# Performance work log

Hardware: AMD Instinct MI355X
Metric: run time of the kernel (lower is better)

The kernel has to match this reference:

```python
import jax, jax.numpy as jnp
import numpy as np
from jax import lax

B, CIN, H, W = 64, 3, 224, 224
FEAT = 64          # conv output channels after pooling
OUT = 1024         # output_dim


def _conv2d(x, w, b, stride):
    # x: NCHW, w: OIHW, padding=1, stride=stride
    y = lax.conv_general_dilated(
        x, w, window_strides=(stride, stride), padding=((1, 1), (1, 1)),
        dimension_numbers=("NCHW", "OIHW", "NCHW"))
    return y + b[None, :, None, None]


def setup_inputs() -> dict:
    key = jax.random.key(0)
    ks = jax.random.split(key, 12)
    s = 0.05
    return {
        "x": jax.random.normal(ks[0], (B, CIN, H, W), dtype=jnp.float32),
        "w1": jax.random.normal(ks[1], (32, CIN, 3, 3), dtype=jnp.float32) * s,
        "b1": jax.random.normal(ks[2], (32,), dtype=jnp.float32) * s,
        "w2": jax.random.normal(ks[3], (64, 32, 3, 3), dtype=jnp.float32) * s,
        "b2": jax.random.normal(ks[4], (64,), dtype=jnp.float32) * s,
        "wm": jax.random.normal(ks[5], (OUT, FEAT), dtype=jnp.float32) * s,
        "bm": jax.random.normal(ks[6], (OUT,), dtype=jnp.float32) * s,
        "wc": jax.random.normal(ks[7], (OUT, FEAT * FEAT), dtype=jnp.float32) * s,
        "bc": jax.random.normal(ks[8], (OUT,), dtype=jnp.float32) * s,
        "w3": jax.random.normal(ks[9], (OUT, FEAT ** 3), dtype=jnp.float32) * s,
        "b3": jax.random.normal(ks[10], (OUT,), dtype=jnp.float32) * s,
    }


def reference(x, w1, b1, w2, b2, wm, bm, wc, bc, w3, b3):
    # conv trunk: conv3x3 s2 -> relu -> conv3x3 s2 -> relu -> global avg pool
    h = jax.nn.relu(_conv2d(x, w1, b1, 2))
    h = jax.nn.relu(_conv2d(h, w2, b2, 2))
    feat = jnp.mean(h, axis=(2, 3))                    # (B, 64)

    mean_feat = feat @ wm.T + bm                       # (B, OUT)

    fc = feat - jnp.mean(feat, axis=1, keepdims=True)  # centered (B, 64)

    # 2nd-order: outer product flattened -> linear
    cov = (fc[:, :, None] * fc[:, None, :]).reshape(B, FEAT * FEAT)
    cov_feat = cov @ wc.T + bc

    # 3rd-order: rank-1 third-order outer product flattened -> linear
    outer3 = (fc[:, :, None, None] * fc[:, None, :, None] * fc[:, None, None, :])
    third_feat = outer3.reshape(B, FEAT ** 3) @ w3.T + b3

    return mean_feat + cov_feat + third_feat
```

## Files before the change

### kernel.cpp

```cpp
#include <hip/hip_runtime.h>
#include <hip/hip_bf16.h>

#define BB   64
#define CIN  3
#define HH   224
#define WW   224
#define C1   32
#define H1   112
#define W1   112
#define C2   64
#define H2   56
#define W2   56
#define FEATN 64
#define OUTN 1024
#define K3TOT (FEATN*FEATN*FEATN)

typedef __bf16 bf16x8 __attribute__((ext_vector_type(8)));
typedef float  f32x4  __attribute__((ext_vector_type(4)));
typedef unsigned int u32;

__device__ __forceinline__ void gload_lds16(const void* g, void* l) {
  __builtin_amdgcn_global_load_lds((const __attribute__((address_space(1))) u32*)g,
                                   (__attribute__((address_space(3))) u32*)l, 16, 0, 0);
}
__device__ __forceinline__ void gload_lds16_nt(const void* g, void* l) {
  __builtin_amdgcn_global_load_lds((const __attribute__((address_space(1))) u32*)g,
                                   (__attribute__((address_space(3))) u32*)l, 16, 0, 2);
}

__global__ __launch_bounds__(256) void prep_kernel(__bf16* __restrict__ h1T,
        const float* __restrict__ w2, __bf16* __restrict__ wf) {
    int gid = blockIdx.x * 256 + threadIdx.x;
    if (gid < 64 * 452) {
      int b = gid / 452, s = gid - b * 452;
      int row, col;
      if      (s < 114) { row = 0;        col = s; }
      else if (s < 228) { row = 113;      col = s - 114; }
      else if (s < 340) { row = s - 227;  col = 0; }
      else              { row = s - 339;  col = 113; }
      __bf16* p = h1T + (((size_t)b * 114 + row) * 114 + col) * 32;
      bf16x8 z = {};
      #pragma unroll
      for (int k = 0; k < 4; ++k) *(bf16x8*)(p + k * 8) = z;
    } else if (gid < 64 * 452 + 18432) {
      int t = gid - 64 * 452;
      int e    = t & 7;
      int lane = (t >> 3) & 63;
      int q    = (t >> 9) % 9;
      int j    = t / 4608;
      int oc = j * 16 + (lane & 15);
      int c  = (lane >> 4) * 8 + e;
      wf[t] = (__bf16)w2[(oc * C1 + c) * 9 + q];
    }
}

__global__ __launch_bounds__(256) void conv1_kernel(const float* __restrict__ x,
        const float* __restrict__ w1, const float* __restrict__ b1,
        __bf16* __restrict__ h1T) {
    int pos = blockIdx.x * 256 + threadIdx.x;
    int b   = pos / (H1 * 56);
    int rem = pos - b * (H1 * 56);
    int oy  = rem / 56;
    int g   = rem - oy * 56;
    int iy0 = oy * 2 - 1;

    float win[CIN][3][5];
    #pragma unroll
    for (int c = 0; c < CIN; ++c)
      #pragma unroll
      for (int dy = 0; dy < 3; ++dy) {
        int iy = iy0 + dy;
        bool rv = (iy >= 0) & (iy < HH);
        const float* row = x + ((size_t)(b * CIN + c) * HH + (rv ? iy : 0)) * WW;
        float lf = (rv && g > 0) ? row[4 * g - 1] : 0.f;
        float4 f4 = rv ? *(const float4*)(row + 4 * g) : (float4){0.f, 0.f, 0.f, 0.f};
        win[c][dy][0] = lf;
        win[c][dy][1] = f4.x; win[c][dy][2] = f4.y;
        win[c][dy][3] = f4.z; win[c][dy][4] = f4.w;
      }

    float acc[2][C1];
    #pragma unroll
    for (int u = 0; u < 2; ++u)
      #pragma unroll
      for (int oc = 0; oc < C1; ++oc) acc[u][oc] = b1[oc];

    #pragma unroll
    for (int c = 0; c < CIN; ++c)
      #pragma unroll
      for (int dy = 0; dy < 3; ++dy)
        #pragma unroll
        for (int dx = 0; dx < 3; ++dx) {
          float w0 = win[c][dy][dx];
          float w1v = win[c][dy][dx + 2];
          const float* wq = w1 + c * 9 + dy * 3 + dx;
          #pragma unroll
          for (int oc = 0; oc < C1; ++oc) {
            float wv = wq[oc * 27];
            acc[0][oc] = fmaf(wv, w0, acc[0][oc]);
            acc[1][oc] = fmaf(wv, w1v, acc[1][oc]);
          }
        }

    __bf16* dst = h1T + (((size_t)b * 114 + oy + 1) * 114 + (2 * g) + 1) * 32;
    #pragma unroll
    for (int u = 0; u < 2; ++u) {
      bf16x8 outv[4];
      #pragma unroll
      for (int k = 0; k < 32; ++k)
        outv[k >> 3][k & 7] = (__bf16)fmaxf(acc[u][k], 0.f);
      #pragma unroll
      for (int k = 0; k < 4; ++k) *(bf16x8*)(dst + u * 32 + k * 8) = outv[k];
    }
}

__global__ __launch_bounds__(256) void conv2_kernel(const __bf16* __restrict__ h1T,
        const __bf16* __restrict__ wf, const float* __restrict__ b2,
        float* __restrict__ featp) {
    __shared__ __align__(16) char tile[2304 * 16];
    __shared__ float pool_red[4][64];
    int t = threadIdx.x;
    int bid = blockIdx.x;
    int b  = bid / 28;
    int yt = bid - b * 28;
    int y0 = yt * 2;
    int w = t >> 6, lane = t & 63, l15 = lane & 15, l4 = lane >> 4;

    const char* src_base = (const char*)(h1T + ((size_t)b * 114 + 2 * y0) * 114 * 32);
    #pragma unroll
    for (int i = 0; i < 9; ++i) {
      int g = (w * 9 + i) * 64 + lane;
      int site = g >> 2; site = site < 569 ? site : 569;
      int qp = g & 3;
      int r5 = site / 114;
      int col = site - r5 * 114;
      int ql = (qp - col) & 3;
      gload_lds16(src_base + (size_t)site * 64 + ql * 16, tile + (size_t)g * 16);
    }
    __syncthreads();

    int sbase[2], urot[2];
    #pragma unroll
    for (int p = 0; p < 2; ++p) {
      int mt = 2 * w + p;
      int yl = mt >> 2;
      int xl = ((mt & 3) << 4) + l15;
      int xe = xl < 55 ? xl : 55;
      sbase[p] = ((yl * 2) * 114 + 2 * xe) * 64;
      urot[p]  = (l4 + 2 * xe) & 3;
    }

    f32x4 acc[2][4];
    #pragma unroll
    for (int p = 0; p < 2; ++p)
      #pragma unroll
      for (int j = 0; j < 4; ++j) acc[p][j] = (f32x4){0.f, 0.f, 0.f, 0.f};

    #pragma unroll
    for (int q = 0; q < 9; ++q) {
      int dy = q / 3, dx = q % 3;
      bf16x8 bw[4];
      #pragma unroll
      for (int j = 0; j < 4; ++j)
        bw[j] = *(const bf16x8*)(wf + ((j * 9 + q) * 64 + lane) * 8);
      bf16x8 af[2];
      #pragma unroll
      for (int p = 0; p < 2; ++p) {
        int addr = sbase[p] + (dy * 114 + dx) * 64 + (((urot[p] + dx) & 3) << 4);
        af[p] = *(const bf16x8*)(tile + addr);
      }
      #pragma unroll
      for (int p = 0; p < 2; ++p)
        #pragma unroll
        for (int j = 0; j < 4; ++j)
          acc[p][j] = __builtin_amdgcn_mfma_f32_16x16x32_bf16(af[p], bw[j], acc[p][j], 0, 0, 0);
    }

    float bias[4];
    #pragma unroll
    for (int j = 0; j < 4; ++j) bias[j] = b2[j * 16 + l15];
    float ps[4] = {0.f, 0.f, 0.f, 0.f};
    #pragma unroll
    for (int p = 0; p < 2; ++p) {
      int mt = 2 * w + p;
      bool valid = ((mt & 3) != 3) || (l4 < 2);
      #pragma unroll
      for (int j = 0; j < 4; ++j) {
        float sj = 0.f;
        #pragma unroll
        for (int r = 0; r < 4; ++r)
          sj += fmaxf(acc[p][j][r] + bias[j], 0.f);
        ps[j] += valid ? sj : 0.f;
      }
    }
    #pragma unroll
    for (int j = 0; j < 4; ++j) {
      ps[j] += __shfl_xor(ps[j], 16);
      ps[j] += __shfl_xor(ps[j], 32);
    }
    if (l4 == 0) {
      #pragma unroll
      for (int j = 0; j < 4; ++j) pool_red[w][j * 16 + l15] = ps[j];
    }
    __syncthreads();
    if (t < 64) {
      float s = pool_red[0][t] + pool_red[1][t] + pool_red[2][t] + pool_red[3][t];
      featp[((size_t)yt * 64 + b) * 64 + t] = s;
    }
}

__global__ __launch_bounds__(64) void center2_kernel(const float* __restrict__ featp,
        float* __restrict__ featN, float* __restrict__ fc) {
    int b = blockIdx.x;
    int c = threadIdx.x;
    float s = 0.f;
    #pragma unroll 7
    for (int yt = 0; yt < 28; ++yt)
      s += featp[((size_t)yt * 64 + b) * 64 + c];
    s *= (1.f / (H2 * W2));
    float tot = s;
    #pragma unroll
    for (int off = 32; off; off >>= 1) tot += __shfl_xor(tot, off);
    featN[b * 64 + c] = s;
    fc[b * 64 + c]    = s - tot * (1.f / 64.f);
}

#define T3_NCH 128

struct T3S {
    float stage[2][2][16][64];
    float fcT[64][66];
    float wred[2][64];
};

__global__ __launch_bounds__(128) void third_kernel(const float* __restrict__ fc,
        const float* __restrict__ w3, float* __restrict__ thrd) {
    __shared__ __align__(16) T3S sh;
    int t = threadIdx.x;
    int w = t >> 6, lane = t & 63, l15 = lane & 15, l4 = lane >> 4;
    int o = blockIdx.x;
    int swz = (l15 & 7) << 4;

    for (int idx = t; idx < 4096; idx += 128)
      sh.fcT[idx & 63][idx >> 6] = fc[idx];

    const char* seg = (const char*)w3 + ((size_t)o << 20) + (size_t)w * 524288;

    #pragma unroll
    for (int ii = 0; ii < 4; ++ii) {
      int row = ii * 4 + (lane >> 4);
      int lo  = (lane & 15) * 16;
      gload_lds16_nt(seg + row * 256 + (lo ^ ((row & 7) << 4)),
                     (char*)&sh.stage[w][0][0][0] + ii * 1024);
    }

    bf16x8 bfrag[2][4];
    #pragma unroll
    for (int ks = 0; ks < 2; ++ks)
      #pragma unroll
      for (int nt = 0; nt < 4; ++nt) {
        const float* p = fc + (nt * 16 + l15) * 64 + ks * 32 + l4 * 8;
        float4 v0 = *(const float4*)p;
        float4 v1 = *(const float4*)(p + 4);
        bfrag[ks][nt][0] = (__bf16)v0.x; bfrag[ks][nt][1] = (__bf16)v0.y;
        bfrag[ks][nt][2] = (__bf16)v0.z; bfrag[ks][nt][3] = (__bf16)v0.w;
        bfrag[ks][nt][4] = (__bf16)v1.x; bfrag[ks][nt][5] = (__bf16)v1.y;
        bfrag[ks][nt][6] = (__bf16)v1.z; bfrag[ks][nt][7] = (__bf16)v1.w;
      }

    __syncthreads();

    float oacc[4] = {0.f, 0.f, 0.f, 0.f};

    #pragma unroll 1
    for (int c = 0; c < T3_NCH; ++c) {
      if (c + 1 < T3_NCH) {
        const char* s2 = seg + (size_t)(c + 1) * 4096;
        char* db = (char*)&sh.stage[w][(c + 1) & 1][0][0];
        #pragma unroll
        for (int ii = 0; ii < 4; ++ii) {
          int row = ii * 4 + (lane >> 4);
          int lo  = (lane & 15) * 16;
          gload_lds16_nt(s2 + row * 256 + (lo ^ ((row & 7) << 4)), db + ii * 1024);
        }
        asm volatile("s_waitcnt vmcnt(4)" ::: "memory");
      } else {
        asm volatile("s_waitcnt vmcnt(0)" ::: "memory");
      }
      __builtin_amdgcn_sched_barrier(0);

      const char* cb = (const char*)&sh.stage[w][c & 1][0][0];
      f32x4 acc[4];
      #pragma unroll
      for (int nt = 0; nt < 4; ++nt) acc[nt] = (f32x4){0.f, 0.f, 0.f, 0.f};
      #pragma unroll
      for (int ks = 0; ks < 2; ++ks) {
        int off0 = l15 * 256 + ((ks * 128 + l4 * 32) ^ swz);
        float4 a0 = *(const float4*)(cb + off0);
        float4 a1 = *(const float4*)(cb + (off0 ^ 16));
        bf16x8 af;
        af[0] = (__bf16)a0.x; af[1] = (__bf16)a0.y;
        af[2] = (__bf16)a0.z; af[3] = (__bf16)a0.w;
        af[4] = (__bf16)a1.x; af[5] = (__bf16)a1.y;
        af[6] = (__bf16)a1.z; af[7] = (__bf16)a1.w;
        #pragma unroll
        for (int nt = 0; nt < 4; ++nt)
          acc[nt] = __builtin_amdgcn_mfma_f32_16x16x32_bf16(af, bfrag[ks][nt], acc[nt], 0, 0, 0);
      }
      int i = w * 32 + (c >> 2);
      #pragma unroll
      for (int nt = 0; nt < 4; ++nt) {
        int b = nt * 16 + l15;
        float s = 0.f;
        #pragma unroll
        for (int r = 0; r < 4; ++r) {
          int j = (c * 16 + l4 * 4 + r) & 63;
          s = fmaf(sh.fcT[j][b], acc[nt][r], s);
        }
        oacc[nt] = fmaf(sh.fcT[i][b], s, oacc[nt]);
      }
    }

    #pragma unroll
    for (int nt = 0; nt < 4; ++nt) {
      oacc[nt] += __shfl_xor(oacc[nt], 16);
      oacc[nt] += __shfl_xor(oacc[nt], 32);
    }
    if (l4 == 0) {
      #pragma unroll
      for (int nt = 0; nt < 4; ++nt) sh.wred[w][nt * 16 + l15] = oacc[nt];
    }
    __syncthreads();
    if (t < 64) thrd[o * 64 + t] = sh.wred[0][t] + sh.wred[1][t];
}

__global__ __launch_bounds__(256) void finale_kernel(const float* __restrict__ feat,
        const float* __restrict__ fc,
        const float* __restrict__ wm, const float* __restrict__ bm,
        const float* __restrict__ wc, const float* __restrict__ bcv,
        const float* __restrict__ b3, const float* __restrict__ thrd,
        float* __restrict__ out) {
    __shared__ float featT[FEATN * FEATN];
    __shared__ float fcT[FEATN * FEATN];
    int t = threadIdx.x;
    for (int i = t; i < FEATN * FEATN; i += 256) {
      int b = i >> 6, c = i & 63;
      featT[c*64 + b] = feat[i];
      fcT[c*64 + b]   = fc[i];
    }
    __syncthreads();

    int b = t & 63;
    int o = blockIdx.x * 4 + (t >> 6);

    float fr[64];
    #pragma unroll
    for (int c4 = 0; c4 < 16; ++c4) {
      float4 v = *(const float4*)(fc + b*64 + c4*4);
      fr[c4*4+0]=v.x; fr[c4*4+1]=v.y; fr[c4*4+2]=v.z; fr[c4*4+3]=v.w;
    }

    float acc = bm[o] + bcv[o] + b3[o];
    #pragma unroll 8
    for (int c = 0; c < FEATN; ++c)
      acc = fmaf(featT[c*64 + b], wm[o*FEATN + c], acc);

    const float* wcrow = wc + (size_t)o * (FEATN * FEATN);
    #pragma unroll 1
    for (int c1 = 0; c1 < 64; ++c1) {
      float a2 = 0.f;
      #pragma unroll
      for (int c2 = 0; c2 < 64; ++c2)
        a2 = fmaf(fr[c2], wcrow[c1*64 + c2], a2);
      acc = fmaf(fcT[c1*64 + b], a2, acc);
    }

    out[b * OUTN + o] = acc + thrd[o * 64 + b];
}

extern "C" void kernel_launch(void* const* d_in, const int* in_sizes, int n_in,
                              void* d_out, int out_size, void* d_ws, size_t ws_size,
                              hipStream_t stream) {
    const float* x   = (const float*)d_in[0];
    const float* w1  = (const float*)d_in[1];
    const float* b1  = (const float*)d_in[2];
    const float* w2  = (const float*)d_in[3];
    const float* b2  = (const float*)d_in[4];
    const float* wm  = (const float*)d_in[5];
    const float* bm  = (const float*)d_in[6];
    const float* wc  = (const float*)d_in[7];
    const float* bcv = (const float*)d_in[8];
    const float* w3  = (const float*)d_in[9];
    const float* b3  = (const float*)d_in[10];
    float* out = (float*)d_out;

    float* ws    = (float*)d_ws;
    __bf16* h1T  = (__bf16*)ws;
    float* featp = ws + 13307904;
    float* featN = ws + 13422592;
    float* fcv   = ws + 13426688;
    float* thrd  = ws + 13430784;
    __bf16* wfrg = (__bf16*)(ws + 13496320);

    prep_kernel   <<<185,  256, 0, stream>>>(h1T, w2, wfrg);
    conv1_kernel  <<<1568, 256, 0, stream>>>(x, w1, b1, h1T);
    conv2_kernel  <<<1792, 256, 0, stream>>>(h1T, wfrg, b2, featp);
    center2_kernel<<<64,   64,  0, stream>>>(featp, featN, fcv);
    third_kernel  <<<1024, 128, 0, stream>>>(fcv, w3, thrd);
    finale_kernel <<<256,  256, 0, stream>>>(featN, fcv, wm, bm, wc, bcv, b3, thrd, out);
}
```

Before: 295.6 us.

## Fuse prep into conv1 and give each third-kernel wave a full output row

The padding-zeroing and w2 fragment prep work moves into conv1_kernel, which removes one kernel launch. The third-order kernel now assigns one output row per wave instead of splitting a row across two waves. Each wave streams 256 chunks of w3, and the cross-wave LDS reduction and __syncthreads go away, so the grid halves to 512 blocks. The risk is fewer blocks and longer serial chains per wave, which may reduce memory-level parallelism on a bandwidth-bound stream.

```diff
diff --git a/kernel.cpp b/kernel.cpp
--- a/kernel.cpp
+++ b/kernel.cpp
@@ -28,9 +28,12 @@
                                    (__attribute__((address_space(3))) u32*)l, 16, 0, 2);
 }
 
-__global__ __launch_bounds__(256) void prep_kernel(__bf16* __restrict__ h1T,
-        const float* __restrict__ w2, __bf16* __restrict__ wf) {
+__global__ __launch_bounds__(256) void conv1_kernel(const float* __restrict__ x,
+        const float* __restrict__ w1, const float* __restrict__ b1,
+        __bf16* __restrict__ h1T, const float* __restrict__ w2,
+        __bf16* __restrict__ wf) {
     int gid = blockIdx.x * 256 + threadIdx.x;
+
     if (gid < 64 * 452) {
       int b = gid / 452, s = gid - b * 452;
       int row, col;
@@ -52,12 +55,8 @@
       int c  = (lane >> 4) * 8 + e;
       wf[t] = (__bf16)w2[(oc * C1 + c) * 9 + q];
     }
-}
-
-__global__ __launch_bounds__(256) void conv1_kernel(const float* __restrict__ x,
-        const float* __restrict__ w1, const float* __restrict__ b1,
-        __bf16* __restrict__ h1T) {
-    int pos = blockIdx.x * 256 + threadIdx.x;
+
+    int pos = gid;
     int b   = pos / (H1 * 56);
     int rem = pos - b * (H1 * 56);
     int oy  = rem / 56;
@@ -225,12 +224,11 @@
     fc[b * 64 + c]    = s - tot * (1.f / 64.f);
 }
 
-#define T3_NCH 128
+#define T3_NCH 256
 
 struct T3S {
     float stage[2][2][16][64];
     float fcT[64][66];
-    float wred[2][64];
 };
 
 __global__ __launch_bounds__(128) void third_kernel(const float* __restrict__ fc,
@@ -238,21 +236,21 @@
     __shared__ __align__(16) T3S sh;
     int t = threadIdx.x;
     int w = t >> 6, lane = t & 63, l15 = lane & 15, l4 = lane >> 4;
-    int o = blockIdx.x;
+    int o = blockIdx.x * 2 + w;
     int swz = (l15 & 7) << 4;
+
+    const char* seg = (const char*)w3 + ((size_t)o << 20);
+
+    #pragma unroll
+    for (int ii = 0; ii < 4; ++ii) {
+      int row = ii * 4 + l4;
+      int lo  = l15 * 16;
+      gload_lds16_nt(seg + row * 256 + (lo ^ ((row & 7) << 4)),
+                     (char*)&sh.stage[w][0][0][0] + ii * 1024);
+    }
 
     for (int idx = t; idx < 4096; idx += 128)
       sh.fcT[idx & 63][idx >> 6] = fc[idx];
-
-    const char* seg = (const char*)w3 + ((size_t)o << 20) + (size_t)w * 524288;
-
-    #pragma unroll
-    for (int ii = 0; ii < 4; ++ii) {
-      int row = ii * 4 + (lane >> 4);
-      int lo  = (lane & 15) * 16;
-      gload_lds16_nt(seg + row * 256 + (lo ^ ((row & 7) << 4)),
-                     (char*)&sh.stage[w][0][0][0] + ii * 1024);
-    }
 
     bf16x8 bfrag[2][4];
     #pragma unroll
@@ -279,8 +277,8 @@
         char* db = (char*)&sh.stage[w][(c + 1) & 1][0][0];
         #pragma unroll
         for (int ii = 0; ii < 4; ++ii) {
-          int row = ii * 4 + (lane >> 4);
-          int lo  = (lane & 15) * 16;
+          int row = ii * 4 + l4;
+          int lo  = l15 * 16;
           gload_lds16_nt(s2 + row * 256 + (lo ^ ((row & 7) << 4)), db + ii * 1024);
         }
         asm volatile("s_waitcnt vmcnt(4)" ::: "memory");
@@ -307,7 +305,7 @@
         for (int nt = 0; nt < 4; ++nt)
           acc[nt] = __builtin_amdgcn_mfma_f32_16x16x32_bf16(af, bfrag[ks][nt], acc[nt], 0, 0, 0);
       }
-      int i = w * 32 + (c >> 2);
+      int i = c >> 2;
       #pragma unroll
       for (int nt = 0; nt < 4; ++nt) {
         int b = nt * 16 + l15;
@@ -328,10 +326,9 @@
     }
     if (l4 == 0) {
       #pragma unroll
-      for (int nt = 0; nt < 4; ++nt) sh.wred[w][nt * 16 + l15] = oacc[nt];
-    }
-    __syncthreads();
-    if (t < 64) thrd[o * 64 + t] = sh.wred[0][t] + sh.wred[1][t];
+      for (int nt = 0; nt < 4; ++nt)
+        thrd[o * 64 + nt * 16 + l15] = oacc[nt];
+    }
 }
 
 __global__ __launch_bounds__(256) void finale_kernel(const float* __restrict__ feat,
@@ -402,10 +399,9 @@
     float* thrd  = ws + 13430784;
     __bf16* wfrg = (__bf16*)(ws + 13496320);
 
-    prep_kernel   <<<185,  256, 0, stream>>>(h1T, w2, wfrg);
-    conv1_kernel  <<<1568, 256, 0, stream>>>(x, w1, b1, h1T);
+    conv1_kernel  <<<1568, 256, 0, stream>>>(x, w1, b1, h1T, w2, wfrg);
     conv2_kernel  <<<1792, 256, 0, stream>>>(h1T, wfrg, b2, featp);
     center2_kernel<<<64,   64,  0, stream>>>(featp, featN, fcv);
-    third_kernel  <<<1024, 128, 0, stream>>>(fcv, w3, thrd);
+    third_kernel  <<<512,  128, 0, stream>>>(fcv, w3, thrd);
     finale_kernel <<<256,  256, 0, stream>>>(featN, fcv, wm, bm, wc, bcv, b3, thrd, out);
 }
```

New measurement: 381.1 us, median of 2. 1.29x slower.
